# Kernel tuning notes

Measured on AMD Instinct MI355X. Metric: run time of the kernel, lower is better.

## Reference

```python
import jax, jax.numpy as jnp
import numpy as np

NS_ITERS = 15
EPS = 1e-6


def _sqrtm(x):
    """Newton-Schulz matrix square root, 15 fixed iterations (Lin & Maji)."""
    dim = x.shape[0]
    norm = jnp.linalg.norm(x)  # Frobenius norm
    Y = x / norm
    I = jnp.eye(dim, dtype=x.dtype)
    Z = I
    for _ in range(NS_ITERS):
        T = 0.5 * (3.0 * I - Z @ Y)
        Y = Y @ T
        Z = T @ Z
    return Y * jnp.sqrt(norm)


def _gram(X):
    a, b = X.shape
    return (X @ X.T + EPS * jnp.eye(a, dtype=X.dtype)) / b


def setup_inputs() -> dict:
    key = jax.random.key(0)
    k1, k2 = jax.random.split(key)
    inp = jax.random.normal(k1, (1, 512, 256, 256), dtype=jnp.float32)
    tgt = jax.random.normal(k2, (1, 512, 256, 256), dtype=jnp.float32)
    return {"input": inp, "target_feature": tgt}


def reference(input, target_feature):
    a, b, c, d = input.shape
    n = a * b
    # --- target statistics (precomputed in __init__ of the torch module) ---
    Xt = target_feature.reshape(n, c * d)
    Mt = Xt.mean(axis=1)                     # [n]
    Gt = _gram(Xt - Mt[:, None])             # [n, n]
    sqrt_Gt = _sqrtm(Gt)                     # [n, n]
    # --- current statistics ---
    X = input.reshape(n, c * d)
    M = X.mean(axis=1)
    G = _gram(X - M[:, None])
    sqrt_G = _sqrtm(G)
    # mse(reduction='sum') on means + Bures/Wasserstein SPD distance
    loss = jnp.sum((M - Mt) ** 2)
    loss = loss + jnp.trace(G + Gt) - 2.0 * jnp.trace(sqrt_G @ sqrt_Gt)
    return loss / b
```

## Files before the change

### kernel.cpp

```cpp
#include <hip/hip_runtime.h>
#include <math.h>

#define KDIM 65536
#define MATF 262144
#define NK 16
#define CHUNK 4096
#define EPSG 1e-6

using bf16x8 = __attribute__((ext_vector_type(8))) __bf16;
using f32x4  = __attribute__((ext_vector_type(4))) float;


__global__ __launch_bounds__(256) void k_means(const float* __restrict__ X,
                                               const float* __restrict__ Xt,
                                               float* __restrict__ M) {
  const int row = blockIdx.x, inp = blockIdx.y;
  const float4* p = (const float4*)((inp ? Xt : X) + (size_t)row * KDIM);
  double s = 0.0;
  for (int i = threadIdx.x; i < KDIM / 4; i += 256) {
    float4 v = p[i];
    s += (double)v.x + (double)v.y + (double)v.z + (double)v.w;
  }
  __shared__ double sm[256];
  sm[threadIdx.x] = s;
  __syncthreads();
  for (int o = 128; o > 0; o >>= 1) {
    if (threadIdx.x < o) sm[threadIdx.x] += sm[threadIdx.x + o];
    __syncthreads();
  }
  if (threadIdx.x == 0) M[inp * 512 + row] = (float)(sm[0] * (1.0 / KDIM));
}

__device__ __forceinline__ void cvt8(float4 a, float4 b, bf16x8& hi, bf16x8& lo) {
  float f[8] = {a.x, a.y, a.z, a.w, b.x, b.y, b.z, b.w};
#pragma unroll
  for (int e = 0; e < 8; ++e) {
    __bf16 h = (__bf16)f[e];
    hi[e] = h;
    lo[e] = (__bf16)(f[e] - (float)h);
  }
}

__global__ __launch_bounds__(256, 2) void k_gram(const float* __restrict__ X,
                                                 const float* __restrict__ Xt,
                                                 float* __restrict__ Gp) {
  int rem = blockIdx.x, ti = 0;
  while (rem >= 4 - ti) { rem -= 4 - ti; ++ti; }
  const int tj = ti + rem;
  const int chunk = blockIdx.y, inp = blockIdx.z;
  const float* __restrict__ A = inp ? Xt : X;
  float* __restrict__ C = Gp + ((size_t)(inp * NK + chunk)) * MATF;
  const bool diag = (ti == tj);

  __shared__ bf16x8 AhV[512], AlV[512], BhV[512], BlV[512];

  const int t = threadIdx.x;
  const int srow = t & 127, skh = t >> 7;
  const int sbase = ((srow >> 4) << 6) + (skh << 5) + (srow & 15);

  const float* pa = A + (size_t)(ti * 128 + srow) * KDIM + (size_t)chunk * CHUNK + skh * 16;
  const float* pb = A + (size_t)(tj * 128 + srow) * KDIM + (size_t)chunk * CHUNK + skh * 16;

  const int wave = t >> 6, lane = t & 63;
  const int wy = (wave >> 1) * 64, wx = (wave & 1) * 64;

  f32x4 acc[4][4];
#pragma unroll
  for (int i = 0; i < 4; ++i)
#pragma unroll
    for (int j = 0; j < 4; ++j) acc[i][j] = (f32x4){0.f, 0.f, 0.f, 0.f};

  for (int ks = 0; ks < CHUNK; ks += 32) {
    {
      float4 v0 = *(const float4*)(pa + ks);
      float4 v1 = *(const float4*)(pa + ks + 4);
      float4 v2 = *(const float4*)(pa + ks + 8);
      float4 v3 = *(const float4*)(pa + ks + 12);
      bf16x8 h, l;
      cvt8(v0, v1, h, l); AhV[sbase] = h; AlV[sbase] = l;
      cvt8(v2, v3, h, l); AhV[sbase + 16] = h; AlV[sbase + 16] = l;
      if (!diag) {
        v0 = *(const float4*)(pb + ks);
        v1 = *(const float4*)(pb + ks + 4);
        v2 = *(const float4*)(pb + ks + 8);
        v3 = *(const float4*)(pb + ks + 12);
        cvt8(v0, v1, h, l); BhV[sbase] = h; BlV[sbase] = l;
        cvt8(v2, v3, h, l); BhV[sbase + 16] = h; BlV[sbase + 16] = l;
      }
    }
    __syncthreads();
    const bf16x8* __restrict__ Bh = diag ? AhV : BhV;
    const bf16x8* __restrict__ Bl = diag ? AlV : BlV;
    bf16x8 ah[4], al[4], bh[4], bl[4];
#pragma unroll
    for (int g = 0; g < 4; ++g) {
      ah[g] = AhV[((wave >> 1) * 4 + g) * 64 + lane];
      al[g] = AlV[((wave >> 1) * 4 + g) * 64 + lane];
      bh[g] = Bh[((wave & 1) * 4 + g) * 64 + lane];
      bl[g] = Bl[((wave & 1) * 4 + g) * 64 + lane];
    }
#pragma unroll
    for (int i = 0; i < 4; ++i)
#pragma unroll
      for (int j = 0; j < 4; ++j) {
        acc[i][j] = __builtin_amdgcn_mfma_f32_16x16x32_bf16(ah[i], bh[j], acc[i][j], 0, 0, 0);
        acc[i][j] = __builtin_amdgcn_mfma_f32_16x16x32_bf16(al[i], bh[j], acc[i][j], 0, 0, 0);
        acc[i][j] = __builtin_amdgcn_mfma_f32_16x16x32_bf16(ah[i], bl[j], acc[i][j], 0, 0, 0);
      }
    __syncthreads();
  }
  const int r4 = (lane >> 4) * 4, fc = lane & 15;
#pragma unroll
  for (int i = 0; i < 4; ++i) {
    const int grow = ti * 128 + wy + i * 16 + r4;
#pragma unroll
    for (int j = 0; j < 4; ++j) {
      const int gcol = tj * 128 + wx + j * 16 + fc;
#pragma unroll
      for (int r = 0; r < 4; ++r)
        C[(size_t)(grow + r) * 512 + gcol] = acc[i][j][r];
    }
  }
}

__global__ __launch_bounds__(256) void k_gfin(const float* __restrict__ Gp,
                                              const float* __restrict__ M,
                                              float* __restrict__ G,
                                              double* __restrict__ S) {
  const int inp = blockIdx.y;
  const int idx = blockIdx.x * 256 + threadIdx.x;
  const int i = idx >> 9, j = idx & 511;
  double n2 = 0.0, tr = 0.0;
  float* g = G + (size_t)inp * MATF;
  if (i <= j) {
    double sum = 0.0;
    const float* p = Gp + (size_t)inp * NK * MATF + idx;
#pragma unroll
    for (int c = 0; c < NK; ++c) sum += (double)p[(size_t)c * MATF];
    sum -= 65536.0 * (double)M[inp * 512 + i] * (double)M[inp * 512 + j];
    if (i == j) sum += EPSG;
    float v = (float)(sum * (1.0 / 65536.0));
    g[idx] = v;
    if (i < j) { g[(size_t)j * 512 + i] = v; n2 = 2.0 * (double)v * (double)v; }
    else       { n2 = (double)v * (double)v; tr = (double)v; }
  }
  __shared__ double s1[256], s2[256];
  s1[threadIdx.x] = n2; s2[threadIdx.x] = tr;
  __syncthreads();
  for (int o = 128; o > 0; o >>= 1) {
    if (threadIdx.x < o) { s1[threadIdx.x] += s1[threadIdx.x + o]; s2[threadIdx.x] += s2[threadIdx.x + o]; }
    __syncthreads();
  }
  if (threadIdx.x == 0) { atomicAdd(&S[inp], s1[0]); atomicAdd(&S[2 + inp], s2[0]); }
}

__global__ __launch_bounds__(256) void k_nsinit(const float* __restrict__ G,
                                                float* __restrict__ Y,
                                                float* __restrict__ Z,
                                                const double* __restrict__ S) {
  const int inp = blockIdx.y;
  const int idx = blockIdx.x * 256 + threadIdx.x;
  const float norm = (float)sqrt(S[inp]);
  Y[(size_t)(inp * 2 + 0) * MATF + idx] = G[(size_t)inp * MATF + idx] / norm;
  Y[(size_t)(inp * 2 + 1) * MATF + idx] = 0.0f;
  Z[(size_t)(inp * 2 + 0) * MATF + idx] = ((idx >> 9) == (idx & 511)) ? 1.0f : 0.0f;
  Z[(size_t)(inp * 2 + 1) * MATF + idx] = 0.0f;
}

__device__ __forceinline__ void gemm_ns(const float* __restrict__ A0, const float* __restrict__ A1,
                                        const float* __restrict__ B0, const float* __restrict__ B1,
                                        const float* __restrict__ E0, const float* __restrict__ E1,
                                        float* __restrict__ C, int k0, int mode) {
  __shared__ __align__(16) float As[64][68];
  __shared__ __align__(16) float Bs[64][68];
  const int t = threadIdx.x;
  const int tx = t & 15, ty = t >> 4;
  const int bi = blockIdx.x, bj = blockIdx.y;
  const int ar = t & 63, akq = t >> 6;
  const int bkr = t >> 2, bcs = (t & 3) * 16;

  const float* pa0 = A0 + (size_t)(bi * 64 + ar) * 512 + k0 + akq * 16;
  const float* pa1 = A1 + (size_t)(bi * 64 + ar) * 512 + k0 + akq * 16;
  const float* pb0 = B0 + (size_t)(k0 + bkr) * 512 + bj * 64 + bcs;
  const float* pb1 = B1 + (size_t)(k0 + bkr) * 512 + bj * 64 + bcs;

  float acc[4][4] = {};
  for (int ks = 0; ks < 256; ks += 64) {
#pragma unroll
    for (int q = 0; q < 4; ++q) {
      float4 va = *(const float4*)(pa0 + ks + q * 4);
      float4 vb = *(const float4*)(pa1 + ks + q * 4);
      const int kk = akq * 16 + q * 4;
      As[kk + 0][ar] = va.x + vb.x; As[kk + 1][ar] = va.y + vb.y;
      As[kk + 2][ar] = va.z + vb.z; As[kk + 3][ar] = va.w + vb.w;
    }
#pragma unroll
    for (int q = 0; q < 4; ++q) {
      float4 va = *(const float4*)(pb0 + (size_t)ks * 512 + q * 4);
      float4 vb = *(const float4*)(pb1 + (size_t)ks * 512 + q * 4);
      va.x += vb.x; va.y += vb.y; va.z += vb.z; va.w += vb.w;
      *(float4*)&Bs[bkr][bcs + q * 4] = va;
    }
    __syncthreads();
#pragma unroll 16
    for (int kk = 0; kk < 64; ++kk) {
      const float4 av = *(const float4*)&As[kk][ty << 2];
      const float4 bv = *(const float4*)&Bs[kk][tx << 2];
      acc[0][0] += av.x * bv.x; acc[0][1] += av.x * bv.y; acc[0][2] += av.x * bv.z; acc[0][3] += av.x * bv.w;
      acc[1][0] += av.y * bv.x; acc[1][1] += av.y * bv.y; acc[1][2] += av.y * bv.z; acc[1][3] += av.y * bv.w;
      acc[2][0] += av.z * bv.x; acc[2][1] += av.z * bv.y; acc[2][2] += av.z * bv.z; acc[2][3] += av.z * bv.w;
      acc[3][0] += av.w * bv.x; acc[3][1] += av.w * bv.y; acc[3][2] += av.w * bv.z; acc[3][3] += av.w * bv.w;
    }
    __syncthreads();
  }
#pragma unroll
  for (int r = 0; r < 4; ++r) {
    const int row = bi * 64 + (ty << 2) + r;
    const size_t off = (size_t)row * 512 + bj * 64 + (tx << 2);
    float4 v = make_float4(acc[r][0], acc[r][1], acc[r][2], acc[r][3]);
    if (mode != 0) {
      v.x *= -0.5f; v.y *= -0.5f; v.z *= -0.5f; v.w *= -0.5f;
      if (mode == 1) {
        float4 e0 = *(const float4*)(E0 + off);
        float4 e1 = *(const float4*)(E1 + off);
        v.x += 1.5f * (e0.x + e1.x); v.y += 1.5f * (e0.y + e1.y);
        v.z += 1.5f * (e0.z + e1.z); v.w += 1.5f * (e0.w + e1.w);
      }
    }
    *(float4*)&C[off] = v;
  }
}

__global__ __launch_bounds__(256) void k_ns_W(const float* __restrict__ Y,
                                              const float* __restrict__ Z,
                                              float* __restrict__ W) {
  const int mat = blockIdx.z >> 1, part = blockIdx.z & 1;
  const float* Zp = Z + (size_t)mat * 2 * MATF;
  const float* Yp = Y + (size_t)mat * 2 * MATF;
  gemm_ns(Zp, Zp + MATF, Yp, Yp + MATF, Yp, Yp,
          W + (size_t)(mat * 2 + part) * MATF, part * 256, 0);
}

__global__ __launch_bounds__(256) void k_ns_YZ(const float* __restrict__ Y,
                                               const float* __restrict__ Z,
                                               const float* __restrict__ W,
                                               float* __restrict__ Yn,
                                               float* __restrict__ Zn) {
  const int mat = blockIdx.z >> 2, which = (blockIdx.z >> 1) & 1, part = blockIdx.z & 1;
  const float* Yp = Y + (size_t)mat * 2 * MATF;
  const float* Zp = Z + (size_t)mat * 2 * MATF;
  const float* Wp = W + (size_t)mat * 2 * MATF;
  const int mode = (part == 0) ? 1 : 2;
  const float *a0, *a1, *b0, *b1, *e0, *e1;
  float* c;
  if (which == 0) {
    a0 = Yp; a1 = Yp + MATF; b0 = Wp; b1 = Wp + MATF; e0 = Yp; e1 = Yp + MATF;
    c = Yn + (size_t)(mat * 2 + part) * MATF;
  } else {
    a0 = Wp; a1 = Wp + MATF; b0 = Zp; b1 = Zp + MATF; e0 = Zp; e1 = Zp + MATF;
    c = Zn + (size_t)(mat * 2 + part) * MATF;
  }
  gemm_ns(a0, a1, b0, b1, e0, e1, c, part * 256, mode);
}

__global__ __launch_bounds__(256) void k_cross(const float* __restrict__ Y,
                                               double* __restrict__ S) {
  const float* YA0 = Y;            const float* YA1 = Y + MATF;
  const float* YB0 = Y + 2 * MATF; const float* YB1 = Y + 3 * MATF;
  const int base = (blockIdx.x * 256 + threadIdx.x) * 4;
  double s = 0.0;
#pragma unroll
  for (int r = 0; r < 4; ++r) {
    const int id = base + r;
    const int i = id >> 9, j = id & 511;
    const int jd = j * 512 + i;
    s += ((double)YA0[id] + (double)YA1[id]) * ((double)YB0[jd] + (double)YB1[jd]);
  }
  __shared__ double sm[256];
  sm[threadIdx.x] = s;
  __syncthreads();
  for (int o = 128; o > 0; o >>= 1) {
    if (threadIdx.x < o) sm[threadIdx.x] += sm[threadIdx.x + o];
    __syncthreads();
  }
  if (threadIdx.x == 0) atomicAdd(&S[4], sm[0]);
}

__global__ __launch_bounds__(256) void k_final(const float* __restrict__ M,
                                               const double* __restrict__ S,
                                               float* __restrict__ out) {
  double s = 0.0;
  for (int i = threadIdx.x; i < 512; i += 256) {
    double d = (double)M[i] - (double)M[512 + i];
    s += d * d;
  }
  __shared__ double sm[256];
  sm[threadIdx.x] = s;
  __syncthreads();
  for (int o = 128; o > 0; o >>= 1) {
    if (threadIdx.x < o) sm[threadIdx.x] += sm[threadIdx.x + o];
    __syncthreads();
  }
  if (threadIdx.x == 0) {
    double scale = sqrt(sqrt(S[0]) * sqrt(S[1]));
    double loss = sm[0] + S[2] + S[3] - 2.0 * scale * S[4];
    out[0] = (float)(loss / 512.0);
  }
}

extern "C" void kernel_launch(void* const* d_in, const int* in_sizes, int n_in,
                              void* d_out, int out_size, void* d_ws, size_t ws_size,
                              hipStream_t stream) {
  const float* X = (const float*)d_in[0];
  const float* Xt = (const float*)d_in[1];
  char* wsb = (char*)d_ws;
  float* Mv = (float*)wsb;
  double* S = (double*)(wsb + 4096);
  float* G = (float*)(wsb + 8192);
  float* big = (float*)(wsb + 8192 + 2 * (size_t)MATF * 4);
  float* Gp = big;
  float* Yb[2] = { big, big + 4 * (size_t)MATF };
  float* Zb[2] = { big + 8 * (size_t)MATF, big + 12 * (size_t)MATF };
  float* W = big + 16 * (size_t)MATF;

  hipMemsetAsync(S, 0, 16 * sizeof(double), stream);
  k_means<<<dim3(512, 2), 256, 0, stream>>>(X, Xt, Mv);
  k_gram<<<dim3(10, NK, 2), 256, 0, stream>>>(X, Xt, Gp);
  k_gfin<<<dim3(1024, 2), 256, 0, stream>>>(Gp, Mv, G, S);
  k_nsinit<<<dim3(1024, 2), 256, 0, stream>>>(G, Yb[0], Zb[0], S);
  int cur = 0;
  for (int it = 0; it < 15; ++it) {
    k_ns_W<<<dim3(8, 8, 4), 256, 0, stream>>>(Yb[cur], Zb[cur], W);
    k_ns_YZ<<<dim3(8, 8, 8), 256, 0, stream>>>(Yb[cur], Zb[cur], W, Yb[1 - cur], Zb[1 - cur]);
    cur ^= 1;
  }
  k_cross<<<dim3(256), 256, 0, stream>>>(Yb[cur], S);
  k_final<<<dim3(1), 256, 0, stream>>>(Mv, S, (float*)d_out);
}
```

Measured before the change: 1.414 ms.

## Move Newton-Schulz GEMMs to split-bf16 MFMA using symmetry, prefetch Gram loads

The fp32 FMA tiled GEMMs in the Newton-Schulz iteration are replaced by a bf16 hi/lo split MFMA kernel. Because every iterate is a polynomial in the symmetric Gram matrix, each product is symmetric, so only the upper-triangular 128x128 tiles are computed and then mirrored. The split-K partial buffers and the summation they needed are dropped. The first iteration is folded into the init kernel, where T is computed directly from Y, so one fewer W GEMM is launched. The Gram kernel gains register prefetch of the next k-slice and uses 32 K-chunks when the workspace allows. The NS launches are now only 10 tiles per matrix, which risks low GPU occupancy, and bf16x3 drops the lo*lo term, giving slightly lower precision than true fp32.

```diff
diff --git a/kernel.cpp b/kernel.cpp
--- a/kernel.cpp
+++ b/kernel.cpp
@@ -3,8 +3,6 @@
 
 #define KDIM 65536
 #define MATF 262144
-#define NK 16
-#define CHUNK 4096
 #define EPSG 1e-6
 
 using bf16x8 = __attribute__((ext_vector_type(8))) __bf16;
@@ -43,13 +41,14 @@
 
 __global__ __launch_bounds__(256, 2) void k_gram(const float* __restrict__ X,
                                                  const float* __restrict__ Xt,
-                                                 float* __restrict__ Gp) {
+                                                 float* __restrict__ Gp, int nk) {
   int rem = blockIdx.x, ti = 0;
   while (rem >= 4 - ti) { rem -= 4 - ti; ++ti; }
   const int tj = ti + rem;
   const int chunk = blockIdx.y, inp = blockIdx.z;
+  const int chunkv = KDIM / nk;
   const float* __restrict__ A = inp ? Xt : X;
-  float* __restrict__ C = Gp + ((size_t)(inp * NK + chunk)) * MATF;
+  float* __restrict__ C = Gp + ((size_t)(inp * nk + chunk)) * MATF;
   const bool diag = (ti == tj);
 
   __shared__ bf16x8 AhV[512], AlV[512], BhV[512], BlV[512];
@@ -58,8 +57,8 @@
   const int srow = t & 127, skh = t >> 7;
   const int sbase = ((srow >> 4) << 6) + (skh << 5) + (srow & 15);
 
-  const float* pa = A + (size_t)(ti * 128 + srow) * KDIM + (size_t)chunk * CHUNK + skh * 16;
-  const float* pb = A + (size_t)(tj * 128 + srow) * KDIM + (size_t)chunk * CHUNK + skh * 16;
+  const float* pa = A + (size_t)(ti * 128 + srow) * KDIM + (size_t)chunk * chunkv + skh * 16;
+  const float* pb = A + (size_t)(tj * 128 + srow) * KDIM + (size_t)chunk * chunkv + skh * 16;
 
   const int wave = t >> 6, lane = t & 63;
   const int wy = (wave >> 1) * 64, wx = (wave & 1) * 64;
@@ -70,25 +69,41 @@
 #pragma unroll
     for (int j = 0; j < 4; ++j) acc[i][j] = (f32x4){0.f, 0.f, 0.f, 0.f};
 
-  for (int ks = 0; ks < CHUNK; ks += 32) {
+  float4 ra0 = *(const float4*)(pa);
+  float4 ra1 = *(const float4*)(pa + 4);
+  float4 ra2 = *(const float4*)(pa + 8);
+  float4 ra3 = *(const float4*)(pa + 12);
+  float4 rb0 = {}, rb1 = {}, rb2 = {}, rb3 = {};
+  if (!diag) {
+    rb0 = *(const float4*)(pb);
+    rb1 = *(const float4*)(pb + 4);
+    rb2 = *(const float4*)(pb + 8);
+    rb3 = *(const float4*)(pb + 12);
+  }
+
+  for (int ks = 0; ks < chunkv; ks += 32) {
     {
-      float4 v0 = *(const float4*)(pa + ks);
-      float4 v1 = *(const float4*)(pa + ks + 4);
-      float4 v2 = *(const float4*)(pa + ks + 8);
-      float4 v3 = *(const float4*)(pa + ks + 12);
       bf16x8 h, l;
-      cvt8(v0, v1, h, l); AhV[sbase] = h; AlV[sbase] = l;
-      cvt8(v2, v3, h, l); AhV[sbase + 16] = h; AlV[sbase + 16] = l;
+      cvt8(ra0, ra1, h, l); AhV[sbase] = h; AlV[sbase] = l;
+      cvt8(ra2, ra3, h, l); AhV[sbase + 16] = h; AlV[sbase + 16] = l;
       if (!diag) {
-        v0 = *(const float4*)(pb + ks);
-        v1 = *(const float4*)(pb + ks + 4);
-        v2 = *(const float4*)(pb + ks + 8);
-        v3 = *(const float4*)(pb + ks + 12);
-        cvt8(v0, v1, h, l); BhV[sbase] = h; BlV[sbase] = l;
-        cvt8(v2, v3, h, l); BhV[sbase + 16] = h; BlV[sbase + 16] = l;
-      }
-    }
-    __syncthreads();
+        cvt8(rb0, rb1, h, l); BhV[sbase] = h; BlV[sbase] = l;
+        cvt8(rb2, rb3, h, l); BhV[sbase + 16] = h; BlV[sbase + 16] = l;
+      }
+    }
+    __syncthreads();
+    if (ks + 32 < chunkv) {
+      ra0 = *(const float4*)(pa + ks + 32);
+      ra1 = *(const float4*)(pa + ks + 36);
+      ra2 = *(const float4*)(pa + ks + 40);
+      ra3 = *(const float4*)(pa + ks + 44);
+      if (!diag) {
+        rb0 = *(const float4*)(pb + ks + 32);
+        rb1 = *(const float4*)(pb + ks + 36);
+        rb2 = *(const float4*)(pb + ks + 40);
+        rb3 = *(const float4*)(pb + ks + 44);
+      }
+    }
     const bf16x8* __restrict__ Bh = diag ? AhV : BhV;
     const bf16x8* __restrict__ Bl = diag ? AlV : BlV;
     bf16x8 ah[4], al[4], bh[4], bl[4];
@@ -126,7 +141,7 @@
 __global__ __launch_bounds__(256) void k_gfin(const float* __restrict__ Gp,
                                               const float* __restrict__ M,
                                               float* __restrict__ G,
-                                              double* __restrict__ S) {
+                                              double* __restrict__ S, int nk) {
   const int inp = blockIdx.y;
   const int idx = blockIdx.x * 256 + threadIdx.x;
   const int i = idx >> 9, j = idx & 511;
@@ -134,9 +149,8 @@
   float* g = G + (size_t)inp * MATF;
   if (i <= j) {
     double sum = 0.0;
-    const float* p = Gp + (size_t)inp * NK * MATF + idx;
-#pragma unroll
-    for (int c = 0; c < NK; ++c) sum += (double)p[(size_t)c * MATF];
+    const float* p = Gp + (size_t)inp * nk * MATF + idx;
+    for (int c = 0; c < nk; ++c) sum += (double)p[(size_t)c * MATF];
     sum -= 65536.0 * (double)M[inp * 512 + i] * (double)M[inp * 512 + j];
     if (i == j) sum += EPSG;
     float v = (float)(sum * (1.0 / 65536.0));
@@ -155,126 +169,146 @@
 }
 
 __global__ __launch_bounds__(256) void k_nsinit(const float* __restrict__ G,
-                                                float* __restrict__ Y,
-                                                float* __restrict__ Z,
+                                                float* __restrict__ Y0,
+                                                float* __restrict__ Z1,
                                                 const double* __restrict__ S) {
   const int inp = blockIdx.y;
   const int idx = blockIdx.x * 256 + threadIdx.x;
   const float norm = (float)sqrt(S[inp]);
-  Y[(size_t)(inp * 2 + 0) * MATF + idx] = G[(size_t)inp * MATF + idx] / norm;
-  Y[(size_t)(inp * 2 + 1) * MATF + idx] = 0.0f;
-  Z[(size_t)(inp * 2 + 0) * MATF + idx] = ((idx >> 9) == (idx & 511)) ? 1.0f : 0.0f;
-  Z[(size_t)(inp * 2 + 1) * MATF + idx] = 0.0f;
-}
-
-__device__ __forceinline__ void gemm_ns(const float* __restrict__ A0, const float* __restrict__ A1,
-                                        const float* __restrict__ B0, const float* __restrict__ B1,
-                                        const float* __restrict__ E0, const float* __restrict__ E1,
-                                        float* __restrict__ C, int k0, int mode) {
-  __shared__ __align__(16) float As[64][68];
-  __shared__ __align__(16) float Bs[64][68];
+  const float y = G[(size_t)inp * MATF + idx] / norm;
+  Y0[(size_t)inp * MATF + idx] = y;
+  Z1[(size_t)inp * MATF + idx] = ((idx >> 9) == (idx & 511)) ? (1.5f - 0.5f * y) : (-0.5f * y);
+}
+
+__device__ __forceinline__ void ns_gemm(const float* __restrict__ A,
+                                        const float* __restrict__ B,
+                                        const float* __restrict__ E,
+                                        float* __restrict__ C, int mode) {
+  int rem = blockIdx.x, ti = 0;
+  while (rem >= 4 - ti) { rem -= 4 - ti; ++ti; }
+  const int tj = ti + rem;
+
+  __shared__ bf16x8 AhV[512], AlV[512], BhV[512], BlV[512];
+
   const int t = threadIdx.x;
-  const int tx = t & 15, ty = t >> 4;
-  const int bi = blockIdx.x, bj = blockIdx.y;
-  const int ar = t & 63, akq = t >> 6;
-  const int bkr = t >> 2, bcs = (t & 3) * 16;
-
-  const float* pa0 = A0 + (size_t)(bi * 64 + ar) * 512 + k0 + akq * 16;
-  const float* pa1 = A1 + (size_t)(bi * 64 + ar) * 512 + k0 + akq * 16;
-  const float* pb0 = B0 + (size_t)(k0 + bkr) * 512 + bj * 64 + bcs;
-  const float* pb1 = B1 + (size_t)(k0 + bkr) * 512 + bj * 64 + bcs;
-
-  float acc[4][4] = {};
-  for (int ks = 0; ks < 256; ks += 64) {
-#pragma unroll
-    for (int q = 0; q < 4; ++q) {
-      float4 va = *(const float4*)(pa0 + ks + q * 4);
-      float4 vb = *(const float4*)(pa1 + ks + q * 4);
-      const int kk = akq * 16 + q * 4;
-      As[kk + 0][ar] = va.x + vb.x; As[kk + 1][ar] = va.y + vb.y;
-      As[kk + 2][ar] = va.z + vb.z; As[kk + 3][ar] = va.w + vb.w;
-    }
-#pragma unroll
-    for (int q = 0; q < 4; ++q) {
-      float4 va = *(const float4*)(pb0 + (size_t)ks * 512 + q * 4);
-      float4 vb = *(const float4*)(pb1 + (size_t)ks * 512 + q * 4);
-      va.x += vb.x; va.y += vb.y; va.z += vb.z; va.w += vb.w;
-      *(float4*)&Bs[bkr][bcs + q * 4] = va;
-    }
-    __syncthreads();
-#pragma unroll 16
-    for (int kk = 0; kk < 64; ++kk) {
-      const float4 av = *(const float4*)&As[kk][ty << 2];
-      const float4 bv = *(const float4*)&Bs[kk][tx << 2];
-      acc[0][0] += av.x * bv.x; acc[0][1] += av.x * bv.y; acc[0][2] += av.x * bv.z; acc[0][3] += av.x * bv.w;
-      acc[1][0] += av.y * bv.x; acc[1][1] += av.y * bv.y; acc[1][2] += av.y * bv.z; acc[1][3] += av.y * bv.w;
-      acc[2][0] += av.z * bv.x; acc[2][1] += av.z * bv.y; acc[2][2] += av.z * bv.z; acc[2][3] += av.z * bv.w;
-      acc[3][0] += av.w * bv.x; acc[3][1] += av.w * bv.y; acc[3][2] += av.w * bv.z; acc[3][3] += av.w * bv.w;
-    }
-    __syncthreads();
-  }
-#pragma unroll
-  for (int r = 0; r < 4; ++r) {
-    const int row = bi * 64 + (ty << 2) + r;
-    const size_t off = (size_t)row * 512 + bj * 64 + (tx << 2);
-    float4 v = make_float4(acc[r][0], acc[r][1], acc[r][2], acc[r][3]);
-    if (mode != 0) {
-      v.x *= -0.5f; v.y *= -0.5f; v.z *= -0.5f; v.w *= -0.5f;
-      if (mode == 1) {
-        float4 e0 = *(const float4*)(E0 + off);
-        float4 e1 = *(const float4*)(E1 + off);
-        v.x += 1.5f * (e0.x + e1.x); v.y += 1.5f * (e0.y + e1.y);
-        v.z += 1.5f * (e0.z + e1.z); v.w += 1.5f * (e0.w + e1.w);
-      }
-    }
-    *(float4*)&C[off] = v;
-  }
-}
-
-__global__ __launch_bounds__(256) void k_ns_W(const float* __restrict__ Y,
-                                              const float* __restrict__ Z,
-                                              float* __restrict__ W) {
-  const int mat = blockIdx.z >> 1, part = blockIdx.z & 1;
-  const float* Zp = Z + (size_t)mat * 2 * MATF;
-  const float* Yp = Y + (size_t)mat * 2 * MATF;
-  gemm_ns(Zp, Zp + MATF, Yp, Yp + MATF, Yp, Yp,
-          W + (size_t)(mat * 2 + part) * MATF, part * 256, 0);
-}
-
-__global__ __launch_bounds__(256) void k_ns_YZ(const float* __restrict__ Y,
-                                               const float* __restrict__ Z,
-                                               const float* __restrict__ W,
-                                               float* __restrict__ Yn,
-                                               float* __restrict__ Zn) {
-  const int mat = blockIdx.z >> 2, which = (blockIdx.z >> 1) & 1, part = blockIdx.z & 1;
-  const float* Yp = Y + (size_t)mat * 2 * MATF;
-  const float* Zp = Z + (size_t)mat * 2 * MATF;
-  const float* Wp = W + (size_t)mat * 2 * MATF;
-  const int mode = (part == 0) ? 1 : 2;
-  const float *a0, *a1, *b0, *b1, *e0, *e1;
-  float* c;
+  const int srow = t & 127, sko = t >> 7;
+  const int sslot = ((srow >> 4) << 6) + (sko << 4) + (srow & 15);
+
+  const float* pa = A + (size_t)(ti * 128 + srow) * 512 + sko * 8;
+  const float* pb = B + (size_t)(tj * 128 + srow) * 512 + sko * 8;
+
+  const int wave = t >> 6, lane = t & 63;
+  const int wy = (wave >> 2) * 64, wx = (wave & 3) * 32;
+
+  f32x4 acc[4][2];
+#pragma unroll
+  for (int i = 0; i < 4; ++i)
+#pragma unroll
+    for (int j = 0; j < 2; ++j) acc[i][j] = (f32x4){0.f, 0.f, 0.f, 0.f};
+
+  float4 ra0 = *(const float4*)(pa), ra1 = *(const float4*)(pa + 4);
+  float4 rb0 = *(const float4*)(pb), rb1 = *(const float4*)(pb + 4);
+
+  for (int ks = 0; ks < 512; ks += 32) {
+    {
+      bf16x8 h, l;
+      cvt8(ra0, ra1, h, l); AhV[sslot] = h; AlV[sslot] = l;
+      cvt8(rb0, rb1, h, l); BhV[sslot] = h; BlV[sslot] = l;
+    }
+    __syncthreads();
+    if (ks + 32 < 512) {
+      ra0 = *(const float4*)(pa + ks + 32); ra1 = *(const float4*)(pa + ks + 36);
+      rb0 = *(const float4*)(pb + ks + 32); rb1 = *(const float4*)(pb + ks + 36);
+    }
+    bf16x8 ah[4], al[4], bh[2], bl[2];
+#pragma unroll
+    for (int g = 0; g < 4; ++g) {
+      ah[g] = AhV[((wy >> 4) + g) * 64 + lane];
+      al[g] = AlV[((wy >> 4) + g) * 64 + lane];
+    }
+#pragma unroll
+    for (int g = 0; g < 2; ++g) {
+      bh[g] = BhV[((wx >> 4) + g) * 64 + lane];
+      bl[g] = BlV[((wx >> 4) + g) * 64 + lane];
+    }
+#pragma unroll
+    for (int i = 0; i < 4; ++i)
+#pragma unroll
+      for (int j = 0; j < 2; ++j) {
+        acc[i][j] = __builtin_amdgcn_mfma_f32_16x16x32_bf16(ah[i], bh[j], acc[i][j], 0, 0, 0);
+        acc[i][j] = __builtin_amdgcn_mfma_f32_16x16x32_bf16(al[i], bh[j], acc[i][j], 0, 0, 0);
+        acc[i][j] = __builtin_amdgcn_mfma_f32_16x16x32_bf16(ah[i], bl[j], acc[i][j], 0, 0, 0);
+      }
+    __syncthreads();
+  }
+
+  const int r4 = (lane >> 4) * 4, fc = lane & 15;
+#pragma unroll
+  for (int i = 0; i < 4; ++i) {
+    const int grow = ti * 128 + wy + i * 16 + r4;
+#pragma unroll
+    for (int j = 0; j < 2; ++j) {
+      const int gcol = tj * 128 + wx + j * 16 + fc;
+      float v[4];
+#pragma unroll
+      for (int r = 0; r < 4; ++r) v[r] = acc[i][j][r];
+      if (mode) {
+#pragma unroll
+        for (int r = 0; r < 4; ++r)
+          v[r] = 1.5f * E[(size_t)(grow + r) * 512 + gcol] - 0.5f * v[r];
+      }
+#pragma unroll
+      for (int r = 0; r < 4; ++r) C[(size_t)(grow + r) * 512 + gcol] = v[r];
+      if (ti != tj) {
+        float4 mv = make_float4(v[0], v[1], v[2], v[3]);
+        *(float4*)&C[(size_t)gcol * 512 + grow] = mv;
+      }
+    }
+  }
+}
+
+__global__ __launch_bounds__(512, 2) void k_ns_first(const float* __restrict__ Y0,
+                                                     float* __restrict__ Y1) {
+  const int mat = blockIdx.y;
+  const float* a = Y0 + (size_t)mat * MATF;
+  ns_gemm(a, a, a, Y1 + (size_t)mat * MATF, 1);
+}
+
+__global__ __launch_bounds__(512, 2) void k_ns_W(const float* __restrict__ Y,
+                                                 const float* __restrict__ Z,
+                                                 float* __restrict__ W) {
+  const int mat = blockIdx.y;
+  ns_gemm(Z + (size_t)mat * MATF, Y + (size_t)mat * MATF, nullptr,
+          W + (size_t)mat * MATF, 0);
+}
+
+__global__ __launch_bounds__(512, 2) void k_ns_YZ(const float* __restrict__ Y,
+                                                  const float* __restrict__ Z,
+                                                  const float* __restrict__ W,
+                                                  float* __restrict__ Yn,
+                                                  float* __restrict__ Zn) {
+  const int mat = blockIdx.y >> 1, which = blockIdx.y & 1;
+  const float* Wp = W + (size_t)mat * MATF;
   if (which == 0) {
-    a0 = Yp; a1 = Yp + MATF; b0 = Wp; b1 = Wp + MATF; e0 = Yp; e1 = Yp + MATF;
-    c = Yn + (size_t)(mat * 2 + part) * MATF;
+    const float* Yp = Y + (size_t)mat * MATF;
+    ns_gemm(Yp, Wp, Yp, Yn + (size_t)mat * MATF, 1);
   } else {
-    a0 = Wp; a1 = Wp + MATF; b0 = Zp; b1 = Zp + MATF; e0 = Zp; e1 = Zp + MATF;
-    c = Zn + (size_t)(mat * 2 + part) * MATF;
-  }
-  gemm_ns(a0, a1, b0, b1, e0, e1, c, part * 256, mode);
+    const float* Zp = Z + (size_t)mat * MATF;
+    ns_gemm(Wp, Zp, Zp, Zn + (size_t)mat * MATF, 1);
+  }
 }
 
 __global__ __launch_bounds__(256) void k_cross(const float* __restrict__ Y,
                                                double* __restrict__ S) {
-  const float* YA0 = Y;            const float* YA1 = Y + MATF;
-  const float* YB0 = Y + 2 * MATF; const float* YB1 = Y + 3 * MATF;
+  const float* YA = Y;
+  const float* YB = Y + MATF;
   const int base = (blockIdx.x * 256 + threadIdx.x) * 4;
   double s = 0.0;
 #pragma unroll
   for (int r = 0; r < 4; ++r) {
     const int id = base + r;
     const int i = id >> 9, j = id & 511;
-    const int jd = j * 512 + i;
-    s += ((double)YA0[id] + (double)YA1[id]) * ((double)YB0[jd] + (double)YB1[jd]);
+    s += (double)YA[id] * (double)YB[j * 512 + i];
   }
   __shared__ double sm[256];
   sm[threadIdx.x] = s;
@@ -318,20 +352,25 @@
   double* S = (double*)(wsb + 4096);
   float* G = (float*)(wsb + 8192);
   float* big = (float*)(wsb + 8192 + 2 * (size_t)MATF * 4);
+
+  const size_t need32 = 8192 + 2 * (size_t)MATF * 4 + 2 * 32 * (size_t)MATF * 4;
+  const int nk = (ws_size >= need32) ? 32 : 16;
+
   float* Gp = big;
-  float* Yb[2] = { big, big + 4 * (size_t)MATF };
-  float* Zb[2] = { big + 8 * (size_t)MATF, big + 12 * (size_t)MATF };
-  float* W = big + 16 * (size_t)MATF;
+  float* Yb[2] = { big, big + 2 * (size_t)MATF };
+  float* Zb[2] = { big + 4 * (size_t)MATF, big + 6 * (size_t)MATF };
+  float* W = big + 8 * (size_t)MATF;
 
   hipMemsetAsync(S, 0, 16 * sizeof(double), stream);
   k_means<<<dim3(512, 2), 256, 0, stream>>>(X, Xt, Mv);
-  k_gram<<<dim3(10, NK, 2), 256, 0, stream>>>(X, Xt, Gp);
-  k_gfin<<<dim3(1024, 2), 256, 0, stream>>>(Gp, Mv, G, S);
-  k_nsinit<<<dim3(1024, 2), 256, 0, stream>>>(G, Yb[0], Zb[0], S);
-  int cur = 0;
-  for (int it = 0; it < 15; ++it) {
-    k_ns_W<<<dim3(8, 8, 4), 256, 0, stream>>>(Yb[cur], Zb[cur], W);
-    k_ns_YZ<<<dim3(8, 8, 8), 256, 0, stream>>>(Yb[cur], Zb[cur], W, Yb[1 - cur], Zb[1 - cur]);
+  k_gram<<<dim3(10, nk, 2), 256, 0, stream>>>(X, Xt, Gp, nk);
+  k_gfin<<<dim3(1024, 2), 256, 0, stream>>>(Gp, Mv, G, S, nk);
+  k_nsinit<<<dim3(1024, 2), 256, 0, stream>>>(G, Yb[0], Zb[1], S);
+  k_ns_first<<<dim3(10, 2), 512, 0, stream>>>(Yb[0], Yb[1]);
+  int cur = 1;
+  for (int it = 1; it < 15; ++it) {
+    k_ns_W<<<dim3(10, 2), 512, 0, stream>>>(Yb[cur], Zb[cur], W);
+    k_ns_YZ<<<dim3(10, 4), 512, 0, stream>>>(Yb[cur], Zb[cur], W, Yb[1 - cur], Zb[1 - cur]);
     cur ^= 1;
   }
   k_cross<<<dim3(256), 256, 0, stream>>>(Yb[cur], S);
```

Result: faster. 1.323 ms (-6.4%).
